# Optimization experiments

Measured on AMD Instinct MI355X. Metric: run time of the kernel, lower is better.

## Reference

```python
import jax, jax.numpy as jnp
import numpy as np

N_NODES = 50000
N_EDGES = 400000
F_IN = 128
HID = 64
HEADS = 8
N_CLASSES = 16
NEG_SLOPE = 0.2  # PyG GATConv default negative_slope


def _glorot(key, shape):
    fan_in, fan_out = shape[0], shape[-1]
    lim = jnp.sqrt(6.0 / (fan_in + fan_out))
    return jax.random.uniform(key, shape, jnp.float32, -lim, lim)


def setup_inputs() -> dict:
    key = jax.random.key(0)
    ks = jax.random.split(key, 16)
    x = jax.random.normal(ks[0], (N_NODES, F_IN), jnp.float32)
    edge_index = jax.random.randint(ks[1], (2, N_EDGES), 0, N_NODES, jnp.int64)
    # layer 0: F_IN -> HEADS*HID (concat)
    W0 = _glorot(ks[2], (F_IN, HEADS * HID))
    a_s0 = _glorot(ks[3], (HEADS, HID))
    a_d0 = _glorot(ks[4], (HEADS, HID))
    b0 = jnp.zeros((HEADS * HID,), jnp.float32)
    # layer 1: HEADS*HID -> HEADS*HID (concat)
    W1 = _glorot(ks[5], (HEADS * HID, HEADS * HID))
    a_s1 = _glorot(ks[6], (HEADS, HID))
    a_d1 = _glorot(ks[7], (HEADS, HID))
    b1 = jnp.zeros((HEADS * HID,), jnp.float32)
    # final layer: HEADS*HID -> N_CLASSES, heads=1, concat=False (mean over heads)
    W2 = _glorot(ks[8], (HEADS * HID, 1 * N_CLASSES))
    a_s2 = _glorot(ks[9], (1, N_CLASSES))
    a_d2 = _glorot(ks[10], (1, N_CLASSES))
    b2 = jnp.zeros((N_CLASSES,), jnp.float32)
    return {"x": x, "edge_index": edge_index,
            "W0": W0, "a_s0": a_s0, "a_d0": a_d0, "b0": b0,
            "W1": W1, "a_s1": a_s1, "a_d1": a_d1, "b1": b1,
            "W2": W2, "a_s2": a_s2, "a_d2": a_d2, "b2": b2}


def gat_conv(x, src, dst, W, a_src, a_dst, b, num_nodes, concat):
    """One PyG-style GATConv (self-loops already in src/dst).
    x: [N, F_in]; W: [F_in, H*C]; a_src/a_dst: [H, C]; b: [H*C] or [C]."""
    H, C = a_src.shape
    h = (x @ W).reshape(num_nodes, H, C)                    # [N,H,C]
    al_s = jnp.einsum('nhc,hc->nh', h, a_src)               # [N,H]
    al_d = jnp.einsum('nhc,hc->nh', h, a_dst)               # [N,H]
    e = jax.nn.leaky_relu(al_s[src] + al_d[dst], NEG_SLOPE) # [E,H]
    # scatter-softmax over incoming edges of each destination node
    m = jax.ops.segment_max(e, dst, num_segments=num_nodes)  # [N,H]
    ex = jnp.exp(e - m[dst])
    denom = jax.ops.segment_sum(ex, dst, num_segments=num_nodes)
    alpha = ex / denom[dst]                                  # [E,H]
    out = jax.ops.segment_sum(alpha[:, :, None] * h[src], dst,
                              num_segments=num_nodes)        # [N,H,C]
    if concat:
        return out.reshape(num_nodes, H * C) + b
    return out.mean(axis=1) + b


def reference(x, edge_index, W0, a_s0, a_d0, b0, W1, a_s1, a_d1, b1,
              W2, a_s2, a_d2, b2):
    N = x.shape[0]
    # PyG GATConv adds self-loops by default
    loops = jnp.arange(N, dtype=edge_index.dtype)
    src = jnp.concatenate([edge_index[0], loops])
    dst = jnp.concatenate([edge_index[1], loops])
    h = gat_conv(x, src, dst, W0, a_s0, a_d0, b0, N, concat=True)
    h = jax.nn.elu(h)  # dropout is identity in eval mode
    h = gat_conv(h, src, dst, W1, a_s1, a_d1, b1, N, concat=True)
    h = jax.nn.elu(h)
    return gat_conv(h, src, dst, W2, a_s2, a_d2, b2, N, concat=False)
```

## Files before the change

kernel.cpp:

```cpp
#include <hip/hip_runtime.h>

#define N_NODES 50000
#define N_EDGES 400000
#define E_TOT   450000
#define NEG 0.2f
#define NB_SCAN ((N_NODES + 255) / 256)
#define MAXD 64
#define NG0 196
#define EPB ((E_TOT + NG0 - 1) / NG0)

typedef unsigned short ushort_t;
typedef __attribute__((ext_vector_type(8))) _Float16 half8;
typedef __attribute__((ext_vector_type(4))) float  f32x4;
typedef __attribute__((ext_vector_type(8))) unsigned short ushort8;

__device__ __forceinline__ ushort_t f2h(float f){
    _Float16 h = (_Float16)f;
    union { _Float16 h; ushort_t u; } v; v.h = h; return v.u;
}
__device__ __forceinline__ float h_lo(unsigned u){
    union { unsigned u; _Float16 h[2]; } v; v.u = u; return (float)v.h[0];
}
__device__ __forceinline__ float h_hi(unsigned u){
    union { unsigned u; _Float16 h[2]; } v; v.u = u; return (float)v.h[1];
}
__device__ __forceinline__ void gload_lds16(const void* g, void* l){
    __builtin_amdgcn_global_load_lds((const __attribute__((address_space(1))) void*)g,
                                     (__attribute__((address_space(3))) void*)l, 16, 0, 0);
}
__device__ __forceinline__ int wave_incl_scan(int v, int lane){
    #pragma unroll
    for(int off = 1; off < 64; off <<= 1){
        int t = __shfl_up(v, off, 64);
        if(lane >= off) v += t;
    }
    return v;
}


__global__ void cvt_all(const float* __restrict__ W0,
                        const float* __restrict__ W1, const float* __restrict__ W2,
                        const int* __restrict__ ei,
                        ushort_t* __restrict__ W0t,
                        ushort_t* __restrict__ W1t, ushort_t* __restrict__ W2t,
                        int* __restrict__ deg){
    int i = blockIdx.x*256 + threadIdx.x;
    if(i < 512*128){ int n = i >> 7, k = i & 127; W0t[i] = f2h(W0[(size_t)k*512 + n]); }
    if(i < 512*512){ int n = i >> 9, k = i & 511; W1t[i] = f2h(W1[(size_t)k*512 + n]); }
    if(i < 16*512){ int n = i >> 9, k = i & 511; W2t[i] = f2h(W2[(size_t)k*16 + n]); }
    if(i < E_TOT){
        int dst = (i < N_EDGES) ? ei[N_EDGES + i] : (i - N_EDGES);
        atomicAdd(&deg[dst], 1);
    }
}


__global__ void deg_block_sum(const int* __restrict__ deg, int* __restrict__ bsum){
    int i = blockIdx.x*256 + threadIdx.x;
    int lane = threadIdx.x & 63, wave = threadIdx.x >> 6;
    int v = (i < N_NODES) ? deg[i] : 0;
    #pragma unroll
    for(int off = 1; off < 64; off <<= 1) v += __shfl_xor(v, off, 64);
    __shared__ int sw[4];
    if(lane == 0) sw[wave] = v;
    __syncthreads();
    if(threadIdx.x == 0) bsum[blockIdx.x] = sw[0] + sw[1] + sw[2] + sw[3];
}

__global__ void scan_apply(const int* __restrict__ bsum,
                           int* __restrict__ dw, int* __restrict__ rowptr){
    __shared__ int soff;
    __shared__ int sw[4];
    int i = blockIdx.x*256 + threadIdx.x;
    int lane = threadIdx.x & 63, wave = threadIdx.x >> 6;
    if(wave == 0){
        int s = 0;
        for(int j = lane; j < (int)blockIdx.x; j += 64) s += bsum[j];
        #pragma unroll
        for(int off = 1; off < 64; off <<= 1) s += __shfl_xor(s, off, 64);
        if(lane == 0) soff = s;
    }
    int v = (i < N_NODES) ? dw[i] : 0;
    int incl = wave_incl_scan(v, lane);
    if(lane == 63) sw[wave] = incl;
    __syncthreads();
    int add = soff;
    for(int w = 0; w < wave; w++) add += sw[w];
    int excl = incl - v + add;
    if(i < N_NODES){ rowptr[i] = excl; dw[i] = excl; }
    if(i == N_NODES-1) rowptr[N_NODES] = excl + v;
}


__global__ __launch_bounds__(512, 1) void gemm0fs(const int* __restrict__ ei,
                                                  int* __restrict__ wofs,
                                                  int* __restrict__ csr,
                                                  const float* __restrict__ x,
                                                  const ushort_t* __restrict__ W0t,
                                                  ushort_t* __restrict__ Cb,
                                                  const float* __restrict__ a_s,
                                                  const float* __restrict__ a_d,
                                                  float* __restrict__ als,
                                                  float* __restrict__ ald, int M){
    extern __shared__ ushort_t lds[];
    ushort_t* Bs = lds;
    ushort_t* As = lds + 512*128;
    int tid = threadIdx.x, wave = tid >> 6, lane = tid & 63;
    int rsub = lane >> 4, c16 = lane & 15;
    int fm = lane & 15, fq = lane >> 4;
    long row0 = (long)blockIdx.x * 256;

    auto stageA = [&](long base){
        #pragma unroll
        for(int t = 0; t < 4; t++){
            int rl = wave*16 + t*4 + rsub;
            long gr = base + rl; gr = gr < M ? gr : M-1;
            const float* ap = x + gr*128 + c16*8;
            f32x4 lo = *(const f32x4*)ap;
            f32x4 hi = *(const f32x4*)(ap + 4);
            union { _Float16 h[8]; half8 v; } u;
            u.h[0] = (_Float16)lo[0]; u.h[1] = (_Float16)lo[1];
            u.h[2] = (_Float16)lo[2]; u.h[3] = (_Float16)lo[3];
            u.h[4] = (_Float16)hi[0]; u.h[5] = (_Float16)hi[1];
            u.h[6] = (_Float16)hi[2]; u.h[7] = (_Float16)hi[3];
            *(half8*)&As[(size_t)rl*128 + (c16 ^ (rl & 7))*8] = u.v;
        }
    };
    auto compute = [&](f32x4 (&acc)[8][4]){
        #pragma unroll
        for(int kt = 0; kt < 4; kt++){
            half8 a[8], b[4];
            #pragma unroll
            for(int mi = 0; mi < 8; mi++){
                int r = mi*16 + fm;
                a[mi] = *(const half8*)&As[(size_t)r*128 + ((kt*4 + fq) ^ (r & 7))*8];
            }
            #pragma unroll
            for(int nj = 0; nj < 4; nj++){
                int r = wave*64 + nj*16 + fm;
                b[nj] = *(const half8*)&Bs[(size_t)r*128 + ((kt*4 + fq) ^ (r & 7))*8];
            }
            #pragma unroll
            for(int mi = 0; mi < 8; mi++)
                #pragma unroll
                for(int nj = 0; nj < 4; nj++)
                    acc[mi][nj] = __builtin_amdgcn_mfma_f32_16x16x32_f16(a[mi], b[nj], acc[mi][nj], 0, 0, 0);
        }
    };
    auto epilogue = [&](f32x4 (&acc)[8][4], long base){
        int head = wave;
        float asv[4], adv[4];
        #pragma unroll
        for(int nj = 0; nj < 4; nj++){
            int c = head*64 + nj*16 + fm;
            asv[nj] = a_s[c]; adv[nj] = a_d[c];
        }
        #pragma unroll
        for(int mi = 0; mi < 8; mi++){
            #pragma unroll
            for(int p2 = 0; p2 < 4; p2++){
                long r = base + mi*16 + fq*4 + p2;
                float ps = 0.f, pd = 0.f;
                if(r < M){
                    ushort_t* cp = &Cb[(size_t)r*512 + head*64 + fm];
                    #pragma unroll
                    for(int nj = 0; nj < 4; nj++){
                        float v = acc[mi][nj][p2];
                        cp[nj*16] = f2h(v);
                        ps += v*asv[nj]; pd += v*adv[nj];
                    }
                }
                #pragma unroll
                for(int off = 1; off < 16; off <<= 1){
                    ps += __shfl_xor(ps, off);
                    pd += __shfl_xor(pd, off);
                }
                if(fm == 0 && r < M){ als[r*8 + head] = ps; ald[r*8 + head] = pd; }
            }
        }
    };

    #pragma unroll
    for(int s = 0; s < 16; s++){
        int rowq = wave*64 + s*4;
        int r = rowq + rsub;
        int sc = c16 ^ (r & 7);
        gload_lds16(W0t + (size_t)r*128 + sc*8, Bs + rowq*128);
    }
    stageA(row0);

    {
        int e1 = blockIdx.x*EPB + EPB; if(e1 > E_TOT) e1 = E_TOT;
        for(int e = blockIdx.x*EPB + tid; e < e1; e += 512){
            int src, dst;
            if(e < N_EDGES){ src = ei[e]; dst = ei[N_EDGES + e]; }
            else { src = dst = e - N_EDGES; }
            int pos = atomicAdd(&wofs[dst], 1);
            csr[pos] = src;
        }
    }

    __syncthreads();

    f32x4 acc[8][4] = {};
    compute(acc);
    __syncthreads();
    stageA(row0 + 128);
    epilogue(acc, row0);
    __syncthreads();

    f32x4 acc2[8][4] = {};
    compute(acc2);
    epilogue(acc2, row0 + 128);
}


template<int K>
__global__ __launch_bounds__(512, 2) void gemm_bt8(const ushort_t* __restrict__ A,
                                                   const ushort_t* __restrict__ Bt,
                                                   ushort_t* __restrict__ Cb,
                                                   const float* __restrict__ a_s,
                                                   const float* __restrict__ a_d,
                                                   float* __restrict__ als,
                                                   float* __restrict__ ald, int M){
    extern __shared__ ushort_t lds[];
    constexpr int NT = K / 64;
    int tid = threadIdx.x, wave = tid >> 6, lane = tid & 63;
    int wm = wave >> 2, wn = wave & 3;

    int s = blockIdx.x, nb = gridDim.x;
    int cc = s & 7, kk = s >> 3;
    int q = nb >> 3, rr = nb & 7;
    int t = (cc < rr ? cc*(q+1) : rr*(q+1) + (cc-rr)*q) + kk;
    int row0 = (t >> 1) * 256;
    int col0 = (t & 1) * 256;

    int lr = lane >> 3;
    int cs8 = ((lane & 7) ^ lr) << 3;
    int arows[4], brows[4];
    #pragma unroll
    for(int i = 0; i < 4; i++){
        int r = row0 + (wave << 5) + (i << 3) + lr;
        arows[i] = r < M ? r : M-1;
        brows[i] = col0 + (wave << 5) + (i << 3) + lr;
    }

    int l15 = lane & 15, fq = lane >> 4;
    int xr = (lane & 7) << 4;
    int xco0 = ((fq << 4)      ) ^ xr;
    int xco1 = (64 | (fq << 4)) ^ xr;

    f32x4 acc[8][4] = {};

    auto stage = [&](int nbuf, int kt, int i){
        ushort_t* la = lds + nbuf*16384 + (wave << 11) + (i << 9);
        ushort_t* lb = lds + 32768 + nbuf*16384 + (wave << 11) + (i << 9);
        gload_lds16(A  + (size_t)arows[i]*K + kt + cs8, la);
        gload_lds16(Bt + (size_t)brows[i]*K + kt + cs8, lb);
    };

    #pragma unroll
    for(int i = 0; i < 4; i++) stage(0, 0, i);
    #pragma unroll
    for(int i = 0; i < 4; i++) stage(1, 64, i);

    for(int it = 0; it < NT; ++it){
        int b = it & 1;
        if(it < NT-1) asm volatile("s_waitcnt vmcnt(8)" ::: "memory");
        else         asm volatile("s_waitcnt vmcnt(0)" ::: "memory");
        __builtin_amdgcn_s_barrier();
        const char* Ac = (const char*)(lds + b*16384);
        const char* Bc = (const char*)(lds + 32768 + b*16384);
        #pragma unroll
        for(int p = 0; p < 4; ++p){
            half8 aF[2][2], bF[4][2];
            #pragma unroll
            for(int m2 = 0; m2 < 2; m2++){
                int ro = (((wm << 7) + (((p << 1) | m2) << 4) + l15)) << 7;
                aF[m2][0] = *(const half8*)(Ac + ro + xco0);
                aF[m2][1] = *(const half8*)(Ac + ro + xco1);
            }
            #pragma unroll
            for(int nj = 0; nj < 4; nj++){
                int ro = (((wn << 6) + (nj << 4) + l15)) << 7;
                bF[nj][0] = *(const half8*)(Bc + ro + xco0);
                bF[nj][1] = *(const half8*)(Bc + ro + xco1);
            }
            if(p == 3) asm volatile("s_waitcnt lgkmcnt(0)" ::: "memory");
            __builtin_amdgcn_s_barrier();
            if(p == 3 && it < NT-2){
                #pragma unroll
                for(int i = 0; i < 4; i++) stage(b, (it + 2) << 6, i);
            }
            __builtin_amdgcn_s_setprio(1);
            #pragma unroll
            for(int m2 = 0; m2 < 2; m2++)
                #pragma unroll
                for(int nj = 0; nj < 4; nj++){
                    acc[(p<<1)|m2][nj] = __builtin_amdgcn_mfma_f32_16x16x32_f16(aF[m2][0], bF[nj][0], acc[(p<<1)|m2][nj], 0, 0, 0);
                    acc[(p<<1)|m2][nj] = __builtin_amdgcn_mfma_f32_16x16x32_f16(aF[m2][1], bF[nj][1], acc[(p<<1)|m2][nj], 0, 0, 0);
                }
            __builtin_amdgcn_s_setprio(0);
            __builtin_amdgcn_s_barrier();
        }
    }

    int head = (col0 >> 6) + wn;
    float asv[4], adv[4];
    #pragma unroll
    for(int nj = 0; nj < 4; nj++){
        int c = (head << 6) + (nj << 4) + l15;
        asv[nj] = a_s[c]; adv[nj] = a_d[c];
    }
    #pragma unroll
    for(int mi = 0; mi < 8; mi++){
        #pragma unroll
        for(int p2 = 0; p2 < 4; p2++){
            int r = row0 + (wm << 7) + (mi << 4) + (fq << 2) + p2;
            float ps = 0.f, pd = 0.f;
            if(r < M){
                ushort_t* cp = &Cb[(size_t)r*512 + (head << 6) + l15];
                #pragma unroll
                for(int nj = 0; nj < 4; nj++){
                    float v = acc[mi][nj][p2];
                    cp[nj << 4] = f2h(v);
                    ps += v*asv[nj]; pd += v*adv[nj];
                }
            }
            #pragma unroll
            for(int off = 1; off < 16; off <<= 1){
                ps += __shfl_xor(ps, off);
                pd += __shfl_xor(pd, off);
            }
            if(l15 == 0 && r < M){ als[r*8 + head] = ps; ald[r*8 + head] = pd; }
        }
    }
}


template<bool F2>
__global__ __launch_bounds__(256) void attn_agg(const ushort_t* __restrict__ h,
        const float* __restrict__ als, const float* __restrict__ ald,
        const int* __restrict__ rowptr, const int* __restrict__ csr,
        const float* __restrict__ bias, ushort_t* __restrict__ out,
        const ushort_t* __restrict__ W2t, const float* __restrict__ a_s2,
        const float* __restrict__ a_d2, float* __restrict__ h2,
        float* __restrict__ als2, float* __restrict__ ald2){
    __shared__ float sex[4][MAXD][8];
    int wv = threadIdx.x >> 6, lane = threadIdx.x & 63;
    int n = blockIdx.x*4 + wv;
    int start = rowptr[n], end = rowptr[n+1];

    int hd = lane & 7, e8 = lane >> 3;
    float aldv = ald[n*8 + hd];
    float lmax = -1e30f;
    for(int idx = start + e8; idx < end; idx += 8){
        int e = idx - start;
        int src = csr[idx];
        float v = als[src*8 + hd] + aldv;
        v = v > 0.f ? v : NEG*v;
        if(e < MAXD) sex[wv][e][hd] = v;
        lmax = fmaxf(lmax, v);
    }
    for(int off = 8; off < 64; off <<= 1) lmax = fmaxf(lmax, __shfl_xor(lmax, off));
    float lsum = 0.f;
    for(int idx = start + e8; idx < end; idx += 8){
        int e = idx - start;
        float v;
        if(e < MAXD) v = sex[wv][e][hd];
        else { int src = csr[idx]; v = als[src*8 + hd] + aldv; v = v > 0.f ? v : NEG*v; }
        float ex = __expf(v - lmax);
        if(e < MAXD) sex[wv][e][hd] = ex;
        lsum += ex;
    }
    for(int off = 8; off < 64; off <<= 1) lsum += __shfl_xor(lsum, off);

    int head = e8;
    float m_all = __shfl(lmax, head);
    float inv   = 1.f / __shfl(lsum, head);
    float aldn  = __shfl(aldv, head);

    float acc[8] = {};

    int cnt = end - start;
    int nmain = cnt < MAXD ? cnt : MAXD;
    int mend = start + nmain;
    int last = mend - 1;
    for(int idx = start; idx < mend; idx += 8){
        int ss[8]; uint4 pp[8]; float ee[8];
        #pragma unroll
        for(int k = 0; k < 8; k++){
            int j = idx + k;
            ss[k] = csr[j <= last ? j : last];
        }
        #pragma unroll
        for(int k = 0; k < 8; k++)
            pp[k] = *(const uint4*)&h[(size_t)ss[k]*512 + lane*8];
        #pragma unroll
        for(int k = 0; k < 8; k++){
            int j = idx + k;
            ee[k] = (j < mend) ? sex[wv][j-start][head] : 0.f;
        }
        #pragma unroll
        for(int k = 0; k < 8; k++){
            acc[0] += ee[k]*h_lo(pp[k].x); acc[1] += ee[k]*h_hi(pp[k].x);
            acc[2] += ee[k]*h_lo(pp[k].y); acc[3] += ee[k]*h_hi(pp[k].y);
            acc[4] += ee[k]*h_lo(pp[k].z); acc[5] += ee[k]*h_hi(pp[k].z);
            acc[6] += ee[k]*h_lo(pp[k].w); acc[7] += ee[k]*h_hi(pp[k].w);
        }
    }
    if(mend < end){
        for(int idx = mend; idx < end; idx++){
            int src = csr[idx];
            float v = als[src*8 + head] + aldn;
            v = v > 0.f ? v : NEG*v;
            float e0 = __expf(v - m_all);
            uint4 p = *(const uint4*)&h[(size_t)src*512 + lane*8];
            acc[0] += e0*h_lo(p.x); acc[1] += e0*h_hi(p.x);
            acc[2] += e0*h_lo(p.y); acc[3] += e0*h_hi(p.y);
            acc[4] += e0*h_lo(p.z); acc[5] += e0*h_hi(p.z);
            acc[6] += e0*h_lo(p.w); acc[7] += e0*h_hi(p.w);
        }
    }

    float vv[8];
    ushort8 o;
    #pragma unroll
    for(int j = 0; j < 8; j++){
        float v = acc[j]*inv + bias[lane*8 + j];
        v = v > 0.f ? v : (__expf(v) - 1.f);
        vv[j] = v;
        o[j] = f2h(v);
    }
    if constexpr (!F2){
        *(ushort8*)&out[(size_t)n*512 + lane*8] = o;
    } else {
        float p[16];
        const ushort_t* wp = W2t + lane*8;
        #pragma unroll
        for(int c = 0; c < 16; c++){
            uint4 w4 = *(const uint4*)(wp + (size_t)c*512);
            p[c] = vv[0]*h_lo(w4.x) + vv[1]*h_hi(w4.x)
                 + vv[2]*h_lo(w4.y) + vv[3]*h_hi(w4.y)
                 + vv[4]*h_lo(w4.z) + vv[5]*h_hi(w4.z)
                 + vv[6]*h_lo(w4.w) + vv[7]*h_hi(w4.w);
        }
        bool b5 = (lane & 32);
        float q8[8];
        #pragma unroll
        for(int i = 0; i < 8; i++){
            float keep = b5 ? p[i+8] : p[i];
            float send = b5 ? p[i]   : p[i+8];
            q8[i] = keep + __shfl_xor(send, 32);
        }
        bool b4 = (lane & 16);
        float q4[4];
        #pragma unroll
        for(int i = 0; i < 4; i++){
            float keep = b4 ? q8[i+4] : q8[i];
            float send = b4 ? q8[i]   : q8[i+4];
            q4[i] = keep + __shfl_xor(send, 16);
        }
        bool b3 = (lane & 8);
        float q2[2];
        #pragma unroll
        for(int i = 0; i < 2; i++){
            float keep = b3 ? q4[i+2] : q4[i];
            float send = b3 ? q4[i]   : q4[i+2];
            q2[i] = keep + __shfl_xor(send, 8);
        }
        bool b2 = (lane & 4);
        float keep = b2 ? q2[1] : q2[0];
        float send = b2 ? q2[0] : q2[1];
        float y = keep + __shfl_xor(send, 4);
        y += __shfl_xor(y, 1);
        y += __shfl_xor(y, 2);
        int c = (lane >> 2) & 15;
        if((lane & 3) == 0) h2[(size_t)n*16 + c] = y;
        float ps = y * a_s2[c], pd = y * a_d2[c];
        ps += __shfl_xor(ps, 4);  pd += __shfl_xor(pd, 4);
        ps += __shfl_xor(ps, 8);  pd += __shfl_xor(pd, 8);
        ps += __shfl_xor(ps, 16); pd += __shfl_xor(pd, 16);
        ps += __shfl_xor(ps, 32); pd += __shfl_xor(pd, 32);
        if(lane == 0){ als2[n] = ps; ald2[n] = pd; }
    }
}

__global__ __launch_bounds__(256) void attn_agg2(const float* __restrict__ h2,
        const float* __restrict__ als, const float* __restrict__ ald,
        const int* __restrict__ rowptr, const int* __restrict__ csr,
        const float* __restrict__ b2, float* __restrict__ out){
    __shared__ float sex2[16][MAXD+1];
    int wv = threadIdx.x >> 6, lane = threadIdx.x & 63;
    int q = lane >> 4, c = lane & 15;
    int slot = wv*4 + q;
    int n = blockIdx.x*16 + slot;
    int start = rowptr[n], end = rowptr[n+1];
    float aldv = ald[n];
    int cnt = end - start;
    int nmain = cnt < MAXD ? cnt : MAXD;
    int mend = start + nmain;

    float lmax = -1e30f;
    for(int idx = start + c; idx < end; idx += 16){
        int e = idx - start;
        float v = als[csr[idx]] + aldv; v = v > 0.f ? v : NEG*v;
        if(e < MAXD) sex2[slot][e] = v;
        lmax = fmaxf(lmax, v);
    }
    #pragma unroll
    for(int off = 1; off < 16; off <<= 1) lmax = fmaxf(lmax, __shfl_xor(lmax, off));
    float lsum = 0.f;
    for(int idx = start + c; idx < end; idx += 16){
        int e = idx - start;
        float v;
        if(e < MAXD) v = sex2[slot][e];
        else { v = als[csr[idx]] + aldv; v = v > 0.f ? v : NEG*v; }
        float ex = __expf(v - lmax);
        if(e < MAXD) sex2[slot][e] = ex;
        lsum += ex;
    }
    #pragma unroll
    for(int off = 1; off < 16; off <<= 1) lsum += __shfl_xor(lsum, off);
    float inv = 1.f / lsum;

    float acc = 0.f;
    for(int idx = start; idx < mend; idx++){
        int src = csr[idx];
        float ex = sex2[slot][idx - start];
        acc += ex * h2[(size_t)src*16 + c];
    }
    for(int idx = mend; idx < end; idx++){
        int src = csr[idx];
        float v = als[src] + aldv; v = v > 0.f ? v : NEG*v;
        acc += __expf(v - lmax) * h2[(size_t)src*16 + c];
    }
    out[(size_t)n*16 + c] = acc*inv + b2[c];
}


extern "C" void kernel_launch(void* const* d_in, const int* in_sizes, int n_in,
                              void* d_out, int out_size, void* d_ws, size_t ws_size,
                              hipStream_t stream) {
    const float* x    = (const float*)d_in[0];
    const int*   ei   = (const int*)  d_in[1];
    const float* W0   = (const float*)d_in[2];
    const float* a_s0 = (const float*)d_in[3];
    const float* a_d0 = (const float*)d_in[4];
    const float* b0   = (const float*)d_in[5];
    const float* W1   = (const float*)d_in[6];
    const float* a_s1 = (const float*)d_in[7];
    const float* a_d1 = (const float*)d_in[8];
    const float* b1   = (const float*)d_in[9];
    const float* W2   = (const float*)d_in[10];
    const float* a_s2 = (const float*)d_in[11];
    const float* a_d2 = (const float*)d_in[12];
    const float* b2   = (const float*)d_in[13];
    float* out = (float*)d_out;

    char* w = (char*)d_ws;
    auto alloc = [&](size_t bytes){ void* p = (void*)w; w += (bytes + 255) & ~(size_t)255; return p; };
    int*      rowptr = (int*)     alloc((N_NODES+1)*sizeof(int));
    int*      wofs   = (int*)     alloc((N_NODES+1)*sizeof(int));
    int*      bsum   = (int*)     alloc(NB_SCAN*sizeof(int));
    int*      csr    = (int*)     alloc(E_TOT*sizeof(int));
    float*    als    = (float*)   alloc((size_t)N_NODES*8*sizeof(float));
    float*    ald    = (float*)   alloc((size_t)N_NODES*8*sizeof(float));
    float*    als2   = (float*)   alloc((size_t)N_NODES*sizeof(float));
    float*    ald2   = (float*)   alloc((size_t)N_NODES*sizeof(float));
    ushort_t* hb     = (ushort_t*)alloc((size_t)N_NODES*512*sizeof(ushort_t));
    ushort_t* hbf    = (ushort_t*)alloc((size_t)N_NODES*512*sizeof(ushort_t));
    ushort_t* W0t    = (ushort_t*)alloc((size_t)512*128*sizeof(ushort_t));
    ushort_t* W1t    = (ushort_t*)alloc((size_t)512*512*sizeof(ushort_t));
    ushort_t* W2t    = (ushort_t*)alloc((size_t)16*512*sizeof(ushort_t));
    float*    h2     = (float*)   alloc((size_t)N_NODES*16*sizeof(float));

    const int NBLK = 2 * ((N_NODES + 255) / 256);

    (void)hipFuncSetAttribute((const void*)gemm_bt8<512>,
                              hipFuncAttributeMaxDynamicSharedMemorySize, 131072);
    (void)hipFuncSetAttribute((const void*)gemm0fs,
                              hipFuncAttributeMaxDynamicSharedMemorySize, 163840);

    hipMemsetAsync(wofs, 0, (N_NODES+1)*sizeof(int), stream);
    cvt_all<<<(E_TOT+255)/256, 256, 0, stream>>>(W0, W1, W2, ei, W0t, W1t, W2t, wofs);

    deg_block_sum<<<NB_SCAN, 256, 0, stream>>>(wofs, bsum);
    scan_apply<<<NB_SCAN, 256, 0, stream>>>(bsum, wofs, rowptr);

    gemm0fs<<<NG0, 512, 163840, stream>>>(ei, wofs, csr, x, W0t, hb, a_s0, a_d0, als, ald, N_NODES);
    attn_agg<false><<<N_NODES/4, 256, 0, stream>>>(hb, als, ald, rowptr, csr, b0, hbf,
                                                   nullptr, nullptr, nullptr, nullptr, nullptr, nullptr);

    gemm_bt8<512><<<NBLK, 512, 131072, stream>>>(hbf, W1t, hb, a_s1, a_d1, als, ald, N_NODES);
    attn_agg<true><<<N_NODES/4, 256, 0, stream>>>(hb, als, ald, rowptr, csr, b1, nullptr,
                                                  W2t, a_s2, a_d2, h2, als2, ald2);

    attn_agg2<<<N_NODES/16, 256, 0, stream>>>(h2, als2, ald2, rowptr, csr, b2, out);
}
```

Before: 407.5 us.

## Halve GEMM k-tile to 32 with new LDS swizzle; use fdot2 for W2 projection

The layer-1 GEMM now stages K-tiles of 32 instead of 64, halving LDS use per block (64 KB instead of 128 KB). It issues one MFMA per fragment pair per step and uses a new XOR swizzle for the narrower rows. The intent is to let two 512-thread blocks fit per CU and cut register pressure from the fragment arrays, at the cost of twice as many pipeline iterations and barriers. Separately, the fused 16-class projection in attn_agg uses packed fp16 fdot2 on the fp16-rounded activations instead of fp32 FMAs, which slightly changes precision.

```diff
diff --git a/kernel.cpp b/kernel.cpp
--- a/kernel.cpp
+++ b/kernel.cpp
@@ -11,6 +11,7 @@
 
 typedef unsigned short ushort_t;
 typedef __attribute__((ext_vector_type(8))) _Float16 half8;
+typedef __attribute__((ext_vector_type(2))) _Float16 half2t;
 typedef __attribute__((ext_vector_type(4))) float  f32x4;
 typedef __attribute__((ext_vector_type(8))) unsigned short ushort8;
 
@@ -224,7 +225,7 @@
                                                    float* __restrict__ als,
                                                    float* __restrict__ ald, int M){
     extern __shared__ ushort_t lds[];
-    constexpr int NT = K / 64;
+    constexpr int NT = K / 32;
     int tid = threadIdx.x, wave = tid >> 6, lane = tid & 63;
     int wm = wave >> 2, wn = wave & 3;
 
@@ -235,71 +236,65 @@
     int row0 = (t >> 1) * 256;
     int col0 = (t & 1) * 256;
 
-    int lr = lane >> 3;
-    int cs8 = ((lane & 7) ^ lr) << 3;
-    int arows[4], brows[4];
-    #pragma unroll
-    for(int i = 0; i < 4; i++){
-        int r = row0 + (wave << 5) + (i << 3) + lr;
+    int lr2 = lane >> 2;
+    int c2  = lane & 3;
+    int sc8 = (c2 ^ ((lr2 >> 1) & 3)) << 3;
+    int arows[2], brows[2];
+    #pragma unroll
+    for(int i = 0; i < 2; i++){
+        int r = row0 + (wave << 5) + (i << 4) + lr2;
         arows[i] = r < M ? r : M-1;
-        brows[i] = col0 + (wave << 5) + (i << 3) + lr;
+        brows[i] = col0 + (wave << 5) + (i << 4) + lr2;
     }
 
     int l15 = lane & 15, fq = lane >> 4;
-    int xr = (lane & 7) << 4;
-    int xco0 = ((fq << 4)      ) ^ xr;
-    int xco1 = (64 | (fq << 4)) ^ xr;
 
     f32x4 acc[8][4] = {};
 
-    auto stage = [&](int nbuf, int kt, int i){
-        ushort_t* la = lds + nbuf*16384 + (wave << 11) + (i << 9);
-        ushort_t* lb = lds + 32768 + nbuf*16384 + (wave << 11) + (i << 9);
-        gload_lds16(A  + (size_t)arows[i]*K + kt + cs8, la);
-        gload_lds16(Bt + (size_t)brows[i]*K + kt + cs8, lb);
+    auto stage = [&](int nbuf, int kt){
+        #pragma unroll
+        for(int i = 0; i < 2; i++){
+            ushort_t* la = lds + nbuf*8192 + ((wave << 5) + (i << 4))*32;
+            ushort_t* lb = lds + 16384 + nbuf*8192 + ((wave << 5) + (i << 4))*32;
+            gload_lds16(A  + (size_t)arows[i]*K + kt + sc8, la);
+            gload_lds16(Bt + (size_t)brows[i]*K + kt + sc8, lb);
+        }
     };
 
-    #pragma unroll
-    for(int i = 0; i < 4; i++) stage(0, 0, i);
-    #pragma unroll
-    for(int i = 0; i < 4; i++) stage(1, 64, i);
+    stage(0, 0);
+    stage(1, 32);
 
     for(int it = 0; it < NT; ++it){
         int b = it & 1;
-        if(it < NT-1) asm volatile("s_waitcnt vmcnt(8)" ::: "memory");
+        if(it < NT-1) asm volatile("s_waitcnt vmcnt(4)" ::: "memory");
         else         asm volatile("s_waitcnt vmcnt(0)" ::: "memory");
         __builtin_amdgcn_s_barrier();
-        const char* Ac = (const char*)(lds + b*16384);
-        const char* Bc = (const char*)(lds + 32768 + b*16384);
+        const char* Ac = (const char*)(lds + b*8192);
+        const char* Bc = (const char*)(lds + 16384 + b*8192);
         #pragma unroll
         for(int p = 0; p < 4; ++p){
-            half8 aF[2][2], bF[4][2];
+            half8 aF[2], bF[4];
             #pragma unroll
             for(int m2 = 0; m2 < 2; m2++){
-                int ro = (((wm << 7) + (((p << 1) | m2) << 4) + l15)) << 7;
-                aF[m2][0] = *(const half8*)(Ac + ro + xco0);
-                aF[m2][1] = *(const half8*)(Ac + ro + xco1);
+                int r = (wm << 7) + (((p << 1) | m2) << 4) + l15;
+                aF[m2] = *(const half8*)(Ac + r*64 + ((fq ^ ((r >> 1) & 3)) << 4));
             }
             #pragma unroll
             for(int nj = 0; nj < 4; nj++){
-                int ro = (((wn << 6) + (nj << 4) + l15)) << 7;
-                bF[nj][0] = *(const half8*)(Bc + ro + xco0);
-                bF[nj][1] = *(const half8*)(Bc + ro + xco1);
+                int r = (wn << 6) + (nj << 4) + l15;
+                bF[nj] = *(const half8*)(Bc + r*64 + ((fq ^ ((r >> 1) & 3)) << 4));
             }
             if(p == 3) asm volatile("s_waitcnt lgkmcnt(0)" ::: "memory");
             __builtin_amdgcn_s_barrier();
             if(p == 3 && it < NT-2){
-                #pragma unroll
-                for(int i = 0; i < 4; i++) stage(b, (it + 2) << 6, i);
+                stage(b, (it + 2) << 5);
             }
             __builtin_amdgcn_s_setprio(1);
             #pragma unroll
             for(int m2 = 0; m2 < 2; m2++)
                 #pragma unroll
-                for(int nj = 0; nj < 4; nj++){
-                    acc[(p<<1)|m2][nj] = __builtin_amdgcn_mfma_f32_16x16x32_f16(aF[m2][0], bF[nj][0], acc[(p<<1)|m2][nj], 0, 0, 0);
-                    acc[(p<<1)|m2][nj] = __builtin_amdgcn_mfma_f32_16x16x32_f16(aF[m2][1], bF[nj][1], acc[(p<<1)|m2][nj], 0, 0, 0);
-                }
+                for(int nj = 0; nj < 4; nj++)
+                    acc[(p<<1)|m2][nj] = __builtin_amdgcn_mfma_f32_16x16x32_f16(aF[m2], bF[nj], acc[(p<<1)|m2][nj], 0, 0, 0);
             __builtin_amdgcn_s_setprio(0);
             __builtin_amdgcn_s_barrier();
         }
@@ -435,15 +430,26 @@
     if constexpr (!F2){
         *(ushort8*)&out[(size_t)n*512 + lane*8] = o;
     } else {
+        union { ushort8 v; uint4 d; } ou; ou.v = o;
         float p[16];
         const ushort_t* wp = W2t + lane*8;
         #pragma unroll
         for(int c = 0; c < 16; c++){
             uint4 w4 = *(const uint4*)(wp + (size_t)c*512);
+#if __has_builtin(__builtin_amdgcn_fdot2)
+            union { unsigned u; half2t h; } wa, wb, wc, wd, oa, ob, oc, od;
+            wa.u = w4.x; wb.u = w4.y; wc.u = w4.z; wd.u = w4.w;
+            oa.u = ou.d.x; ob.u = ou.d.y; oc.u = ou.d.z; od.u = ou.d.w;
+            float tq = __builtin_amdgcn_fdot2(wa.h, oa.h, 0.f, false);
+            tq = __builtin_amdgcn_fdot2(wb.h, ob.h, tq, false);
+            tq = __builtin_amdgcn_fdot2(wc.h, oc.h, tq, false);
+            p[c] = __builtin_amdgcn_fdot2(wd.h, od.h, tq, false);
+#else
             p[c] = vv[0]*h_lo(w4.x) + vv[1]*h_hi(w4.x)
                  + vv[2]*h_lo(w4.y) + vv[3]*h_hi(w4.y)
                  + vv[4]*h_lo(w4.z) + vv[5]*h_hi(w4.z)
                  + vv[6]*h_lo(w4.w) + vv[7]*h_hi(w4.w);
+#endif
         }
         bool b5 = (lane & 32);
         float q8[8];
@@ -578,7 +584,7 @@
     const int NBLK = 2 * ((N_NODES + 255) / 256);
 
     (void)hipFuncSetAttribute((const void*)gemm_bt8<512>,
-                              hipFuncAttributeMaxDynamicSharedMemorySize, 131072);
+                              hipFuncAttributeMaxDynamicSharedMemorySize, 65536);
     (void)hipFuncSetAttribute((const void*)gemm0fs,
                               hipFuncAttributeMaxDynamicSharedMemorySize, 163840);
 
@@ -592,7 +598,7 @@
     attn_agg<false><<<N_NODES/4, 256, 0, stream>>>(hb, als, ald, rowptr, csr, b0, hbf,
                                                    nullptr, nullptr, nullptr, nullptr, nullptr, nullptr);
 
-    gemm_bt8<512><<<NBLK, 512, 131072, stream>>>(hbf, W1t, hb, a_s1, a_d1, als, ald, N_NODES);
+    gemm_bt8<512><<<NBLK, 512, 65536, stream>>>(hbf, W1t, hb, a_s1, a_d1, als, ald, N_NODES);
     attn_agg<true><<<N_NODES/4, 256, 0, stream>>>(hb, als, ald, rowptr, csr, b1, nullptr,
                                                   W2t, a_s2, a_d2, h2, als2, ald2);
 
```

Measured after the change: 416.8 us. 2.3% more time.
